# Kernel tuning notes

Hardware: AMD Instinct MI355X
Metric: run time of the kernel (lower is better)

Reference implementation:

```python
import jax, jax.numpy as jnp
import numpy as np

VOCABS = (30000, 20000, 10000, 8000, 5000, 30000, 20000, 10000)
OUT_LEN = 30000
D = 512
H = 4
DK = D // H
N_LAYERS = 4
DFF = 4 * D
BAT = 2048
S = 8


def _layernorm(x, a, b, eps=1e-6):
    # Annotated-transformer LayerNorm: a*(x-mean)/(std+eps)+b, unbiased std (torch default)
    mu = jnp.mean(x, axis=-1, keepdims=True)
    sd = jnp.std(x, axis=-1, ddof=1, keepdims=True)
    return a * (x - mu) / (sd + eps) + b


def setup_inputs() -> dict:
    key = jax.random.key(0)
    ks = jax.random.split(key, 32)
    sc = 0.02
    inp = {
        'sentence': jax.random.randint(ks[0], (BAT, S), 0, min(VOCABS)),
        'mask': jnp.ones((BAT, S), jnp.float32),
        'maskedIndex': jax.random.randint(ks[1], (BAT,), 0, S),
        # padded embedding tables (tied with decoder weights): [n_cols, OUT_LEN, D]
        'emb': jax.random.normal(ks[2], (S, OUT_LEN, D), jnp.float32) * sc,
        'dec_bias': jnp.zeros((S, OUT_LEN), jnp.float32),
        'Wq': jax.random.normal(ks[3], (N_LAYERS, D, D), jnp.float32) * sc,
        'bq': jnp.zeros((N_LAYERS, D), jnp.float32),
        'Wk': jax.random.normal(ks[4], (N_LAYERS, D, D), jnp.float32) * sc,
        'bk': jnp.zeros((N_LAYERS, D), jnp.float32),
        'Wv': jax.random.normal(ks[5], (N_LAYERS, D, D), jnp.float32) * sc,
        'bv': jnp.zeros((N_LAYERS, D), jnp.float32),
        'Wo': jax.random.normal(ks[6], (N_LAYERS, D, D), jnp.float32) * sc,
        'bo': jnp.zeros((N_LAYERS, D), jnp.float32),
        'W1': jax.random.normal(ks[7], (N_LAYERS, D, DFF), jnp.float32) * sc,
        'b1': jnp.zeros((N_LAYERS, DFF), jnp.float32),
        'W2': jax.random.normal(ks[8], (N_LAYERS, DFF, D), jnp.float32) * sc,
        'b2': jnp.zeros((N_LAYERS, D), jnp.float32),
        'ln1_a': jnp.ones((N_LAYERS, D), jnp.float32),
        'ln1_b': jnp.zeros((N_LAYERS, D), jnp.float32),
        'ln2_a': jnp.ones((N_LAYERS, D), jnp.float32),
        'ln2_b': jnp.zeros((N_LAYERS, D), jnp.float32),
        'fn_a': jnp.ones((D,), jnp.float32),
        'fn_b': jnp.zeros((D,), jnp.float32),
    }
    return inp


def reference(sentence, mask, maskedIndex, emb, dec_bias, Wq, bq, Wk, bk, Wv, bv,
              Wo, bo, W1, b1, W2, b2, ln1_a, ln1_b, ln2_a, ln2_b, fn_a, fn_b):
    B = sentence.shape[0]
    # per-column embedding lookup then concat along seq dim -> [B, S, D]
    x = jnp.stack([emb[k][sentence[:, k]] for k in range(S)], axis=1)
    # sinusoidal positional encoding (dropout p=0)
    pos = jnp.arange(S, dtype=jnp.float32)[:, None]
    div = jnp.exp(jnp.arange(0, D, 2, dtype=jnp.float32) * (-np.log(10000.0) / D))
    pe = jnp.zeros((S, D), jnp.float32)
    pe = pe.at[:, 0::2].set(jnp.sin(pos * div)).at[:, 1::2].set(jnp.cos(pos * div))
    x = x + pe[None]
    # mask: [B,S] -> unsqueeze(-1) -> unsqueeze(1) => [B,1,S,1], broadcast vs [B,h,S,S]
    mask_b = (mask[:, None, :, None] == 0)
    scale = 1.0 / np.sqrt(DK)
    for i in range(N_LAYERS):  # pre-LN encoder layers
        h = _layernorm(x, ln1_a[i], ln1_b[i])
        q = (h @ Wq[i] + bq[i]).reshape(B, S, H, DK)
        k = (h @ Wk[i] + bk[i]).reshape(B, S, H, DK)
        v = (h @ Wv[i] + bv[i]).reshape(B, S, H, DK)
        scores = jnp.einsum('bqhd,bkhd->bhqk', q, k) * scale
        scores = jnp.where(mask_b, -1e9, scores)
        p = jax.nn.softmax(scores, axis=-1)
        att = jnp.einsum('bhqk,bkhd->bqhd', p, v).reshape(B, S, D)
        x = x + att @ Wo[i] + bo[i]
        h2 = _layernorm(x, ln2_a[i], ln2_b[i])
        x = x + jax.nn.relu(h2 @ W1[i] + b1[i]) @ W2[i] + b2[i]
    out = _layernorm(x, fn_a, fn_b)
    # per-sample masked-token decode with tied embedding weights, -inf pad to OUT_LEN
    hsel = out[jnp.arange(B), maskedIndex]  # [B, D]
    neg = jnp.float32(-jnp.inf)
    preds = jnp.full((B, OUT_LEN), neg, dtype=out.dtype)
    for kc in range(S):
        vk = VOCABS[kc]
        logits = hsel @ emb[kc, :vk].T + dec_bias[kc, :vk]  # [B, vk]
        if vk < OUT_LEN:
            logits = jnp.concatenate(
                [logits, jnp.full((B, OUT_LEN - vk), neg, out.dtype)], axis=1)
        preds = jnp.where((maskedIndex == kc)[:, None], logits, preds)
    return preds
```

## Files before the change

### kernel.cpp

```cpp
#include <hip/hip_runtime.h>
#include <cstdint>

#define B_   2048
#define S_   8
#define D_   512
#define H_   4
#define DK_  128
#define NL_  4
#define DFF_ 2048
#define OUT_ 30000
#define SENTINEL_ (-1.0e30f)

typedef unsigned short ushort_t;
typedef __attribute__((ext_vector_type(8))) short bf16x8;
typedef __attribute__((ext_vector_type(4))) float f32x4;

__constant__ int VOC_[8] = {30000, 20000, 10000, 8000, 5000, 30000, 20000, 10000};

__device__ __forceinline__ ushort_t f2bf(float f) {
    union { float f; unsigned u; } x; x.f = f;
    unsigned r = x.u + 0x7fffu + ((x.u >> 16) & 1u);
    return (ushort_t)(r >> 16);
}
__device__ __forceinline__ float bf2f(ushort_t h) {
    union { unsigned u; float f; } x; x.u = (unsigned)h << 16;
    return x.f;
}

__global__ __launch_bounds__(256) void convw_k(const float* __restrict__ W,
                                               ushort_t* __restrict__ Wt,
                                               int K, int N) {
    const size_t mat = (size_t)K * N;
    const float* Wz = W + (size_t)blockIdx.z * mat;
    ushort_t* Wtz = Wt + (size_t)blockIdx.z * mat;
    __shared__ __align__(16) ushort_t t[32][40];
    int tid = threadIdx.x;
    int k0 = blockIdx.y * 32, n0 = blockIdx.x * 32;
    int r = tid >> 3, c4 = (tid & 7) * 4;
    float4 v = *(const float4*)(Wz + (size_t)(k0 + r) * N + n0 + c4);
    t[c4 + 0][r] = f2bf(v.x);
    t[c4 + 1][r] = f2bf(v.y);
    t[c4 + 2][r] = f2bf(v.z);
    t[c4 + 3][r] = f2bf(v.w);
    __syncthreads();
    int n = tid >> 3, q = tid & 7;
    uint2 d = *(uint2*)&t[n][q * 4];
    *(uint2*)(Wtz + (size_t)(n0 + n) * K + k0 + q * 4) = d;
}

__global__ __launch_bounds__(128) void embed_pe(const int* __restrict__ sent,
                                                const float* __restrict__ emb,
                                                float* __restrict__ x) {
    int row = blockIdx.x;
    int s = row & 7;
    int tok = sent[row];
    const float* e = emb + ((size_t)s * OUT_ + tok) * D_;
    int d0 = threadIdx.x * 4;
    float4 v = *(const float4*)(e + d0);
    float r[4] = {v.x, v.y, v.z, v.w};
#pragma unroll
    for (int i = 0; i < 4; ++i) {
        int d = d0 + i;
        int i2 = d & ~1;
        float dv = expf((float)i2 * (-9.210340371976184f / 512.f));
        float ang = (float)s * dv;
        r[i] += (d & 1) ? cosf(ang) : sinf(ang);
    }
    *(float4*)(x + (size_t)row * D_ + d0) = make_float4(r[0], r[1], r[2], r[3]);
}

__global__ __launch_bounds__(256) void layernorm_k(const float* __restrict__ x,
                                                   const float* __restrict__ ga,
                                                   const float* __restrict__ gb,
                                                   ushort_t* __restrict__ out) {
    int row  = blockIdx.x * 4 + (threadIdx.x >> 6);
    int lane = threadIdx.x & 63;
    const float* xr = x + (size_t)row * D_;
    float4 v0 = *(const float4*)(xr + lane * 8);
    float4 v1 = *(const float4*)(xr + lane * 8 + 4);
    float s = v0.x + v0.y + v0.z + v0.w + v1.x + v1.y + v1.z + v1.w;
#pragma unroll
    for (int m = 1; m < 64; m <<= 1) s += __shfl_xor(s, m);
    float mu = s * (1.f / 512.f);
    float d0 = v0.x - mu, d1 = v0.y - mu, d2 = v0.z - mu, d3 = v0.w - mu;
    float d4 = v1.x - mu, d5 = v1.y - mu, d6 = v1.z - mu, d7 = v1.w - mu;
    float sq = d0*d0 + d1*d1 + d2*d2 + d3*d3 + d4*d4 + d5*d5 + d6*d6 + d7*d7;
#pragma unroll
    for (int m = 1; m < 64; m <<= 1) sq += __shfl_xor(sq, m);
    float sd  = sqrtf(sq * (1.f / 511.f));
    float inv = 1.f / (sd + 1e-6f);
    float4 a0 = *(const float4*)(ga + lane * 8);
    float4 a1 = *(const float4*)(ga + lane * 8 + 4);
    float4 b0 = *(const float4*)(gb + lane * 8);
    float4 b1 = *(const float4*)(gb + lane * 8 + 4);
    ushort_t u[8];
    u[0] = f2bf(a0.x * d0 * inv + b0.x);  u[1] = f2bf(a0.y * d1 * inv + b0.y);
    u[2] = f2bf(a0.z * d2 * inv + b0.z);  u[3] = f2bf(a0.w * d3 * inv + b0.w);
    u[4] = f2bf(a1.x * d4 * inv + b1.x);  u[5] = f2bf(a1.y * d5 * inv + b1.y);
    u[6] = f2bf(a1.z * d6 * inv + b1.z);  u[7] = f2bf(a1.w * d7 * inv + b1.w);
    *(uint4*)(out + (size_t)row * D_ + lane * 8) = *(uint4*)u;
}

__global__ __launch_bounds__(256) void hsel_ln_k(const float* __restrict__ x,
                                                 const int* __restrict__ mi,
                                                 const float* __restrict__ ga,
                                                 const float* __restrict__ gb,
                                                 ushort_t* __restrict__ hsel) {
    int b    = blockIdx.x * 4 + (threadIdx.x >> 6);
    int lane = threadIdx.x & 63;
    const float* xr = x + ((size_t)b * S_ + mi[b]) * D_;
    float4 v0 = *(const float4*)(xr + lane * 8);
    float4 v1 = *(const float4*)(xr + lane * 8 + 4);
    float s = v0.x + v0.y + v0.z + v0.w + v1.x + v1.y + v1.z + v1.w;
#pragma unroll
    for (int m = 1; m < 64; m <<= 1) s += __shfl_xor(s, m);
    float mu = s * (1.f / 512.f);
    float d0 = v0.x - mu, d1 = v0.y - mu, d2 = v0.z - mu, d3 = v0.w - mu;
    float d4 = v1.x - mu, d5 = v1.y - mu, d6 = v1.z - mu, d7 = v1.w - mu;
    float sq = d0*d0 + d1*d1 + d2*d2 + d3*d3 + d4*d4 + d5*d5 + d6*d6 + d7*d7;
#pragma unroll
    for (int m = 1; m < 64; m <<= 1) sq += __shfl_xor(sq, m);
    float sd  = sqrtf(sq * (1.f / 511.f));
    float inv = 1.f / (sd + 1e-6f);
    float4 a0 = *(const float4*)(ga + lane * 8);
    float4 a1 = *(const float4*)(ga + lane * 8 + 4);
    float4 b0 = *(const float4*)(gb + lane * 8);
    float4 b1 = *(const float4*)(gb + lane * 8 + 4);
    ushort_t u[8];
    u[0] = f2bf(a0.x * d0 * inv + b0.x);  u[1] = f2bf(a0.y * d1 * inv + b0.y);
    u[2] = f2bf(a0.z * d2 * inv + b0.z);  u[3] = f2bf(a0.w * d3 * inv + b0.w);
    u[4] = f2bf(a1.x * d4 * inv + b1.x);  u[5] = f2bf(a1.y * d5 * inv + b1.y);
    u[6] = f2bf(a1.z * d6 * inv + b1.z);  u[7] = f2bf(a1.w * d7 * inv + b1.w);
    *(uint4*)(hsel + (size_t)b * D_ + lane * 8) = *(uint4*)u;
}

template<int RELU, int ACCF32>
__global__ __launch_bounds__(256) void gemm_bt(const ushort_t* __restrict__ A,
                                               const ushort_t* __restrict__ Bt,
                                               const float* __restrict__ bias,
                                               float* __restrict__ Cf,
                                               ushort_t* __restrict__ Cb,
                                               int M, int N, int K) {
    __shared__ __align__(16) ushort_t As[128][40];
    __shared__ __align__(16) ushort_t Bs[128][40];
    const int tid = threadIdx.x;
    const int m0 = blockIdx.y * 128, n0 = blockIdx.x * 128;
    const int lane = tid & 63, w = tid >> 6;
    const int wm = (w >> 1) * 64, wn = (w & 1) * 64;
    const int l15 = lane & 15, kg = lane >> 4;
    f32x4 acc[4][4] = {};
    for (int k0 = 0; k0 < K; k0 += 32) {
        __syncthreads();
#pragma unroll
        for (int it = 0; it < 2; ++it) {
            int lin = tid + it * 256;
            int r = lin >> 2, q = lin & 3;
            *(uint4*)&As[r][q * 8] =
                *(const uint4*)(A + (size_t)(m0 + r) * K + k0 + q * 8);
            *(uint4*)&Bs[r][q * 8] =
                *(const uint4*)(Bt + (size_t)(n0 + r) * K + k0 + q * 8);
        }
        __syncthreads();
        bf16x8 af[4], bfr[4];
#pragma unroll
        for (int m = 0; m < 4; ++m)
            af[m] = *(const bf16x8*)&As[wm + m * 16 + l15][kg * 8];
#pragma unroll
        for (int n = 0; n < 4; ++n)
            bfr[n] = *(const bf16x8*)&Bs[wn + n * 16 + l15][kg * 8];
#pragma unroll
        for (int m = 0; m < 4; ++m)
#pragma unroll
            for (int n = 0; n < 4; ++n)
                acc[m][n] = __builtin_amdgcn_mfma_f32_16x16x32_bf16(
                    af[m], bfr[n], acc[m][n], 0, 0, 0);
    }
#pragma unroll
    for (int n = 0; n < 4; ++n) {
        int col = n0 + wn + n * 16 + l15;
        float bv = bias[col];
#pragma unroll
        for (int m = 0; m < 4; ++m) {
            int rbase = m0 + wm + m * 16 + kg * 4;
#pragma unroll
            for (int r = 0; r < 4; ++r) {
                float v = acc[m][n][r] + bv;
                if (RELU) v = fmaxf(v, 0.f);
                size_t idx = (size_t)(rbase + r) * N + col;
                if (ACCF32) Cf[idx] += v;
                else        Cb[idx] = f2bf(v);
            }
        }
    }
}

__global__ __launch_bounds__(256) void attn_k(const ushort_t* __restrict__ q,
                                              const ushort_t* __restrict__ k,
                                              const ushort_t* __restrict__ v,
                                              const float* __restrict__ mask,
                                              ushort_t* __restrict__ att) {
    int b = blockIdx.x;
    __shared__ float qs[S_][D_], ks[S_][D_], vs[S_][D_];
    __shared__ float ps[H_][S_][S_];
    const int tid = threadIdx.x;
#pragma unroll
    for (int it = 0; it < 2; ++it) {
        int lin = tid + it * 256;
        int s = lin >> 6, d8 = (lin & 63) * 8;
        size_t g = ((size_t)b * S_ + s) * D_ + d8;
        union { uint4 u4; ushort_t u[8]; } uq, uk, uv;
        uq.u4 = *(const uint4*)(q + g);
        uk.u4 = *(const uint4*)(k + g);
        uv.u4 = *(const uint4*)(v + g);
#pragma unroll
        for (int i = 0; i < 8; ++i) {
            qs[s][d8 + i] = bf2f(uq.u[i]);
            ks[s][d8 + i] = bf2f(uk.u[i]);
            vs[s][d8 + i] = bf2f(uv.u[i]);
        }
    }
    __syncthreads();
    const int hh = tid >> 6, lane = tid & 63;
    const int qq = lane >> 3, kk = lane & 7;
    const int off = hh * DK_;
    float s = 0.f;
#pragma unroll
    for (int d = 0; d < DK_; ++d) s = fmaf(qs[qq][off + d], ks[kk][off + d], s);
    s *= 0.08838834764831845f;
    if (mask[b * S_ + qq] == 0.f) s = -1e9f;
    float mx = s;
#pragma unroll
    for (int m = 1; m < 8; m <<= 1) mx = fmaxf(mx, __shfl_xor(mx, m, 8));
    float e = expf(s - mx);
    float sum = e;
#pragma unroll
    for (int m = 1; m < 8; m <<= 1) sum += __shfl_xor(sum, m, 8);
    ps[hh][qq][kk] = e / sum;
    __syncthreads();
#pragma unroll
    for (int q2 = 0; q2 < 8; ++q2) {
        float a0 = 0.f, a1 = 0.f;
#pragma unroll
        for (int k2 = 0; k2 < 8; ++k2) {
            float p = ps[hh][q2][k2];
            a0 = fmaf(p, vs[k2][off + lane], a0);
            a1 = fmaf(p, vs[k2][off + 64 + lane], a1);
        }
        size_t g = ((size_t)b * S_ + q2) * D_ + off;
        att[g + lane]      = f2bf(a0);
        att[g + 64 + lane] = f2bf(a1);
    }
}

__global__ __launch_bounds__(256) void compact_k(const int* __restrict__ mi,
                                                 int* __restrict__ idxg,
                                                 int* __restrict__ off) {
    __shared__ int cnt[8], pos[9];
    int tid = threadIdx.x;
    if (tid < 8) cnt[tid] = 0;
    __syncthreads();
    for (int i = tid; i < B_; i += 256) atomicAdd(&cnt[mi[i]], 1);
    __syncthreads();
    if (tid == 0) {
        pos[0] = 0;
        for (int kc = 0; kc < 8; ++kc) pos[kc + 1] = pos[kc] + cnt[kc];
        for (int kc = 0; kc < 9; ++kc) off[kc] = pos[kc];
    }
    __syncthreads();
    if (tid < 8) cnt[tid] = pos[tid];
    __syncthreads();
    for (int i = tid; i < B_; i += 256) {
        int p = atomicAdd(&cnt[mi[i]], 1);
        idxg[p] = i;
    }
}

__global__ __launch_bounds__(256) void decode_mfma(const ushort_t* __restrict__ hselb,
                                                   const float* __restrict__ emb,
                                                   const float* __restrict__ dbias,
                                                   const int* __restrict__ idxg,
                                                   const int* __restrict__ offg,
                                                   float* __restrict__ out) {
    const int kc = blockIdx.y;
    const int base = offg[kc];
    const int Mg = offg[kc + 1] - base;
    const int m0 = blockIdx.z * 256;
    if (m0 >= Mg) return;
    const int j0 = blockIdx.x * 64;
    const int vk = VOC_[kc];
    const int tid = threadIdx.x;
    const int lane = tid & 63, w = tid >> 6;
    const int l15 = lane & 15, kg = lane >> 4;
    const int wm = w * 64;
    const float* et = emb + (size_t)kc * OUT_ * D_;
    __shared__ __align__(16) ushort_t As[256][40];
    __shared__ __align__(16) ushort_t Bs[64][40];
    f32x4 acc[4][4] = {};
    const bool act = (j0 < vk);
    if (act) {
        for (int k0 = 0; k0 < 512; k0 += 32) {
            __syncthreads();
#pragma unroll
            for (int it = 0; it < 4; ++it) {
                int lin = tid + it * 256;
                int r = lin >> 2, qq = lin & 3;
                uint4 va = make_uint4(0u, 0u, 0u, 0u);
                int m = m0 + r;
                if (m < Mg) {
                    int gb = idxg[base + m];
                    va = *(const uint4*)(hselb + (size_t)gb * D_ + k0 + qq * 8);
                }
                *(uint4*)&As[r][qq * 8] = va;
            }
            {
                int j = tid >> 2, qq = tid & 3;
                int jj = j0 + j; if (jj >= vk) jj = vk - 1;
                const float* src = et + (size_t)jj * D_ + k0 + qq * 8;
                float4 f0 = *(const float4*)src;
                float4 f1 = *(const float4*)(src + 4);
                ushort_t u[8] = {f2bf(f0.x), f2bf(f0.y), f2bf(f0.z), f2bf(f0.w),
                                 f2bf(f1.x), f2bf(f1.y), f2bf(f1.z), f2bf(f1.w)};
                *(uint4*)&Bs[j][qq * 8] = *(uint4*)u;
            }
            __syncthreads();
            bf16x8 af[4], bfr[4];
#pragma unroll
            for (int m = 0; m < 4; ++m)
                af[m] = *(const bf16x8*)&As[wm + m * 16 + l15][kg * 8];
#pragma unroll
            for (int n = 0; n < 4; ++n)
                bfr[n] = *(const bf16x8*)&Bs[n * 16 + l15][kg * 8];
#pragma unroll
            for (int m = 0; m < 4; ++m)
#pragma unroll
                for (int n = 0; n < 4; ++n)
                    acc[m][n] = __builtin_amdgcn_mfma_f32_16x16x32_bf16(
                        af[m], bfr[n], acc[m][n], 0, 0, 0);
        }
    }
#pragma unroll
    for (int m = 0; m < 4; ++m) {
        int rbase = m0 + wm + m * 16 + kg * 4;
#pragma unroll
        for (int r = 0; r < 4; ++r) {
            int mm = rbase + r;
            if (mm >= Mg) continue;
            int b = idxg[base + mm];
            float* orow = out + (size_t)b * OUT_;
#pragma unroll
            for (int n = 0; n < 4; ++n) {
                int col = j0 + n * 16 + l15;
                if (col >= OUT_) continue;
                float v = SENTINEL_;
                if (act && col < vk)
                    v = acc[m][n][r] + dbias[kc * OUT_ + col];
                orow[col] = v;
            }
        }
    }
}

extern "C" void kernel_launch(void* const* d_in, const int* in_sizes, int n_in,
                              void* d_out, int out_size, void* d_ws, size_t ws_size,
                              hipStream_t stream) {
    const int*   sent  = (const int*)d_in[0];
    const float* mask  = (const float*)d_in[1];
    const int*   mi    = (const int*)d_in[2];
    const float* emb   = (const float*)d_in[3];
    const float* dbias = (const float*)d_in[4];
    const float* Wq = (const float*)d_in[5],  *bq = (const float*)d_in[6];
    const float* Wk = (const float*)d_in[7],  *bk = (const float*)d_in[8];
    const float* Wv = (const float*)d_in[9],  *bv = (const float*)d_in[10];
    const float* Wo = (const float*)d_in[11], *bo = (const float*)d_in[12];
    const float* W1 = (const float*)d_in[13], *b1 = (const float*)d_in[14];
    const float* W2 = (const float*)d_in[15], *b2 = (const float*)d_in[16];
    const float* ln1_a = (const float*)d_in[17], *ln1_b = (const float*)d_in[18];
    const float* ln2_a = (const float*)d_in[19], *ln2_b = (const float*)d_in[20];
    const float* fn_a  = (const float*)d_in[21], *fn_b  = (const float*)d_in[22];
    float* out = (float*)d_out;

    const size_t NX = (size_t)B_ * S_ * D_;
    char* p = (char*)d_ws;
    float*    x     = (float*)p;      p += NX * 4;
    ushort_t* h     = (ushort_t*)p;   p += NX * 2;
    ushort_t* reg   = (ushort_t*)p;   p += 4 * NX * 2;
    ushort_t* qb2   = reg;
    ushort_t* kb2   = reg + NX;
    ushort_t* vb2   = reg + 2 * NX;
    ushort_t* ffn1  = reg;
    const size_t WSQ = (size_t)NL_ * D_ * D_;
    const size_t WFF = (size_t)NL_ * D_ * DFF_;
    ushort_t* WqT = (ushort_t*)p;  p += WSQ * 2;
    ushort_t* WkT = (ushort_t*)p;  p += WSQ * 2;
    ushort_t* WvT = (ushort_t*)p;  p += WSQ * 2;
    ushort_t* WoT = (ushort_t*)p;  p += WSQ * 2;
    ushort_t* W1T = (ushort_t*)p;  p += WFF * 2;
    ushort_t* W2T = (ushort_t*)p;  p += WFF * 2;
    ushort_t* hselb = (ushort_t*)p; p += (size_t)B_ * D_ * 2;
    int* idxg = (int*)p;  p += B_ * 4;
    int* offg = (int*)p;

    const int ROWS = B_ * S_;

    convw_k<<<dim3(16, 16, NL_), 256, 0, stream>>>(Wq, WqT, D_, D_);
    convw_k<<<dim3(16, 16, NL_), 256, 0, stream>>>(Wk, WkT, D_, D_);
    convw_k<<<dim3(16, 16, NL_), 256, 0, stream>>>(Wv, WvT, D_, D_);
    convw_k<<<dim3(16, 16, NL_), 256, 0, stream>>>(Wo, WoT, D_, D_);
    convw_k<<<dim3(64, 16, NL_), 256, 0, stream>>>(W1, W1T, D_, DFF_);
    convw_k<<<dim3(16, 64, NL_), 256, 0, stream>>>(W2, W2T, DFF_, D_);

    embed_pe<<<ROWS, 128, 0, stream>>>(sent, emb, x);

    for (int L = 0; L < NL_; ++L) {
        layernorm_k<<<ROWS / 4, 256, 0, stream>>>(x, ln1_a + L * D_, ln1_b + L * D_, h);
        gemm_bt<0, 0><<<dim3(D_ / 128, ROWS / 128), 256, 0, stream>>>(
            h, WqT + (size_t)L * D_ * D_, bq + L * D_, nullptr, qb2, ROWS, D_, D_);
        gemm_bt<0, 0><<<dim3(D_ / 128, ROWS / 128), 256, 0, stream>>>(
            h, WkT + (size_t)L * D_ * D_, bk + L * D_, nullptr, kb2, ROWS, D_, D_);
        gemm_bt<0, 0><<<dim3(D_ / 128, ROWS / 128), 256, 0, stream>>>(
            h, WvT + (size_t)L * D_ * D_, bv + L * D_, nullptr, vb2, ROWS, D_, D_);
        attn_k<<<B_, 256, 0, stream>>>(qb2, kb2, vb2, mask, h);
        gemm_bt<0, 1><<<dim3(D_ / 128, ROWS / 128), 256, 0, stream>>>(
            h, WoT + (size_t)L * D_ * D_, bo + L * D_, x, nullptr, ROWS, D_, D_);
        layernorm_k<<<ROWS / 4, 256, 0, stream>>>(x, ln2_a + L * D_, ln2_b + L * D_, h);
        gemm_bt<1, 0><<<dim3(DFF_ / 128, ROWS / 128), 256, 0, stream>>>(
            h, W1T + (size_t)L * D_ * DFF_, b1 + L * DFF_, nullptr, ffn1, ROWS, DFF_, D_);
        gemm_bt<0, 1><<<dim3(D_ / 128, ROWS / 128), 256, 0, stream>>>(
            ffn1, W2T + (size_t)L * DFF_ * D_, b2 + L * D_, x, nullptr, ROWS, D_, DFF_);
    }

    hsel_ln_k<<<B_ / 4, 256, 0, stream>>>(x, mi, fn_a, fn_b, hselb);
    compact_k<<<1, 256, 0, stream>>>(mi, idxg, offg);
    decode_mfma<<<dim3((OUT_ + 63) / 64, 8, 2), 256, 0, stream>>>(
        hselb, emb, dbias, idxg, offg, out);
}
```

Before: 2.036 ms.

## Fuse QKV GEMMs, use direct global-to-LDS loads, pre-gather decode rows

Concatenates the Q, K and V weights and biases so one GEMM with N=1536 writes an interleaved qkv buffer that attention reads directly. It replaces register-staged tile loads in the GEMM and decode kernels with global_load_lds into unpadded LDS tiles. The final layernorm now writes hidden rows already grouped by column through a rank array, so decode can load A tiles directly. Decode also prefetches the next embedding chunk into registers. Dropping the LDS padding may add bank conflicts on the fragment reads, and it adds a small bias-fusion kernel.

```diff
diff --git a/kernel.cpp b/kernel.cpp
--- a/kernel.cpp
+++ b/kernel.cpp
@@ -27,12 +27,15 @@
     return x.f;
 }
 
+#define GLOAD_LDS16(g, l) __builtin_amdgcn_global_load_lds( \
+    (const __attribute__((address_space(1))) void*)(g),     \
+    (__attribute__((address_space(3))) void*)(l), 16, 0, 0)
+
 __global__ __launch_bounds__(256) void convw_k(const float* __restrict__ W,
                                                ushort_t* __restrict__ Wt,
-                                               int K, int N) {
-    const size_t mat = (size_t)K * N;
-    const float* Wz = W + (size_t)blockIdx.z * mat;
-    ushort_t* Wtz = Wt + (size_t)blockIdx.z * mat;
+                                               int K, int N, size_t ostride) {
+    const float* Wz = W + (size_t)blockIdx.z * K * N;
+    ushort_t* Wtz = Wt + (size_t)blockIdx.z * ostride;
     __shared__ __align__(16) ushort_t t[32][40];
     int tid = threadIdx.x;
     int k0 = blockIdx.y * 32, n0 = blockIdx.x * 32;
@@ -46,6 +49,18 @@
     int n = tid >> 3, q = tid & 7;
     uint2 d = *(uint2*)&t[n][q * 4];
     *(uint2*)(Wtz + (size_t)(n0 + n) * K + k0 + q * 4) = d;
+}
+
+__global__ __launch_bounds__(256) void biasfuse_k(const float* __restrict__ bq,
+                                                  const float* __restrict__ bk,
+                                                  const float* __restrict__ bv,
+                                                  float* __restrict__ o) {
+    int i = blockIdx.x * 256 + threadIdx.x;
+    int L = i / 1536, c = i % 1536;
+    float v = (c < 512) ? bq[L * 512 + c]
+            : (c < 1024) ? bk[L * 512 + c - 512]
+                         : bv[L * 512 + c - 1024];
+    o[i] = v;
 }
 
 __global__ __launch_bounds__(128) void embed_pe(const int* __restrict__ sent,
@@ -103,9 +118,10 @@
 
 __global__ __launch_bounds__(256) void hsel_ln_k(const float* __restrict__ x,
                                                  const int* __restrict__ mi,
+                                                 const int* __restrict__ rank,
                                                  const float* __restrict__ ga,
                                                  const float* __restrict__ gb,
-                                                 ushort_t* __restrict__ hsel) {
+                                                 ushort_t* __restrict__ hselg) {
     int b    = blockIdx.x * 4 + (threadIdx.x >> 6);
     int lane = threadIdx.x & 63;
     const float* xr = x + ((size_t)b * S_ + mi[b]) * D_;
@@ -131,7 +147,7 @@
     u[2] = f2bf(a0.z * d2 * inv + b0.z);  u[3] = f2bf(a0.w * d3 * inv + b0.w);
     u[4] = f2bf(a1.x * d4 * inv + b1.x);  u[5] = f2bf(a1.y * d5 * inv + b1.y);
     u[6] = f2bf(a1.z * d6 * inv + b1.z);  u[7] = f2bf(a1.w * d7 * inv + b1.w);
-    *(uint4*)(hsel + (size_t)b * D_ + lane * 8) = *(uint4*)u;
+    *(uint4*)(hselg + (size_t)rank[b] * D_ + lane * 8) = *(uint4*)u;
 }
 
 template<int RELU, int ACCF32>
@@ -141,33 +157,34 @@
                                                float* __restrict__ Cf,
                                                ushort_t* __restrict__ Cb,
                                                int M, int N, int K) {
-    __shared__ __align__(16) ushort_t As[128][40];
-    __shared__ __align__(16) ushort_t Bs[128][40];
+    __shared__ __align__(16) ushort_t As[128 * 32];
+    __shared__ __align__(16) ushort_t Bs[128 * 32];
     const int tid = threadIdx.x;
     const int m0 = blockIdx.y * 128, n0 = blockIdx.x * 128;
     const int lane = tid & 63, w = tid >> 6;
     const int wm = (w >> 1) * 64, wn = (w & 1) * 64;
     const int l15 = lane & 15, kg = lane >> 4;
+    const int srow = tid >> 2, scq8 = (tid & 3) * 8;
+    const ushort_t* ga0 = A  + (size_t)(m0 + srow) * K + scq8;
+    const ushort_t* gb0 = Bt + (size_t)(n0 + srow) * K + scq8;
+    ushort_t* lA0 = As + w * 64 * 8;
+    ushort_t* lB0 = Bs + w * 64 * 8;
     f32x4 acc[4][4] = {};
     for (int k0 = 0; k0 < K; k0 += 32) {
         __syncthreads();
 #pragma unroll
         for (int it = 0; it < 2; ++it) {
-            int lin = tid + it * 256;
-            int r = lin >> 2, q = lin & 3;
-            *(uint4*)&As[r][q * 8] =
-                *(const uint4*)(A + (size_t)(m0 + r) * K + k0 + q * 8);
-            *(uint4*)&Bs[r][q * 8] =
-                *(const uint4*)(Bt + (size_t)(n0 + r) * K + k0 + q * 8);
+            GLOAD_LDS16(ga0 + (size_t)it * 64 * K + k0, lA0 + it * 2048);
+            GLOAD_LDS16(gb0 + (size_t)it * 64 * K + k0, lB0 + it * 2048);
         }
         __syncthreads();
         bf16x8 af[4], bfr[4];
 #pragma unroll
         for (int m = 0; m < 4; ++m)
-            af[m] = *(const bf16x8*)&As[wm + m * 16 + l15][kg * 8];
+            af[m] = *(const bf16x8*)(As + (wm + m * 16 + l15) * 32 + kg * 8);
 #pragma unroll
         for (int n = 0; n < 4; ++n)
-            bfr[n] = *(const bf16x8*)&Bs[wn + n * 16 + l15][kg * 8];
+            bfr[n] = *(const bf16x8*)(Bs + (wn + n * 16 + l15) * 32 + kg * 8);
 #pragma unroll
         for (int m = 0; m < 4; ++m)
 #pragma unroll
@@ -194,9 +211,7 @@
     }
 }
 
-__global__ __launch_bounds__(256) void attn_k(const ushort_t* __restrict__ q,
-                                              const ushort_t* __restrict__ k,
-                                              const ushort_t* __restrict__ v,
+__global__ __launch_bounds__(256) void attn_k(const ushort_t* __restrict__ qkv,
                                               const float* __restrict__ mask,
                                               ushort_t* __restrict__ att) {
     int b = blockIdx.x;
@@ -207,11 +222,11 @@
     for (int it = 0; it < 2; ++it) {
         int lin = tid + it * 256;
         int s = lin >> 6, d8 = (lin & 63) * 8;
-        size_t g = ((size_t)b * S_ + s) * D_ + d8;
+        size_t rb = ((size_t)b * S_ + s) * 1536 + d8;
         union { uint4 u4; ushort_t u[8]; } uq, uk, uv;
-        uq.u4 = *(const uint4*)(q + g);
-        uk.u4 = *(const uint4*)(k + g);
-        uv.u4 = *(const uint4*)(v + g);
+        uq.u4 = *(const uint4*)(qkv + rb);
+        uk.u4 = *(const uint4*)(qkv + rb + 512);
+        uv.u4 = *(const uint4*)(qkv + rb + 1024);
 #pragma unroll
         for (int i = 0; i < 8; ++i) {
             qs[s][d8 + i] = bf2f(uq.u[i]);
@@ -254,6 +269,7 @@
 
 __global__ __launch_bounds__(256) void compact_k(const int* __restrict__ mi,
                                                  int* __restrict__ idxg,
+                                                 int* __restrict__ rank,
                                                  int* __restrict__ off) {
     __shared__ int cnt[8], pos[9];
     int tid = threadIdx.x;
@@ -272,10 +288,11 @@
     for (int i = tid; i < B_; i += 256) {
         int p = atomicAdd(&cnt[mi[i]], 1);
         idxg[p] = i;
-    }
-}
-
-__global__ __launch_bounds__(256) void decode_mfma(const ushort_t* __restrict__ hselb,
+        rank[i] = p;
+    }
+}
+
+__global__ __launch_bounds__(256) void decode_mfma(const ushort_t* __restrict__ hselg,
                                                    const float* __restrict__ emb,
                                                    const float* __restrict__ dbias,
                                                    const int* __restrict__ idxg,
@@ -292,44 +309,40 @@
     const int lane = tid & 63, w = tid >> 6;
     const int l15 = lane & 15, kg = lane >> 4;
     const int wm = w * 64;
-    const float* et = emb + (size_t)kc * OUT_ * D_;
-    __shared__ __align__(16) ushort_t As[256][40];
-    __shared__ __align__(16) ushort_t Bs[64][40];
+    __shared__ __align__(16) ushort_t As[256 * 32];
+    __shared__ __align__(16) ushort_t Bs[64 * 32];
     f32x4 acc[4][4] = {};
     const bool act = (j0 < vk);
     if (act) {
+        const int srow = tid >> 2, scq8 = (tid & 3) * 8;
+        const ushort_t* gA0 = hselg + (size_t)(base + m0 + srow) * D_ + scq8;
+        ushort_t* lA0 = As + w * 64 * 8;
+        int jj = j0 + srow; if (jj >= vk) jj = vk - 1;
+        const float* gB = emb + ((size_t)kc * OUT_ + jj) * D_ + scq8;
+        float4 e0 = *(const float4*)(gB);
+        float4 e1 = *(const float4*)(gB + 4);
         for (int k0 = 0; k0 < 512; k0 += 32) {
             __syncthreads();
 #pragma unroll
-            for (int it = 0; it < 4; ++it) {
-                int lin = tid + it * 256;
-                int r = lin >> 2, qq = lin & 3;
-                uint4 va = make_uint4(0u, 0u, 0u, 0u);
-                int m = m0 + r;
-                if (m < Mg) {
-                    int gb = idxg[base + m];
-                    va = *(const uint4*)(hselb + (size_t)gb * D_ + k0 + qq * 8);
-                }
-                *(uint4*)&As[r][qq * 8] = va;
+            for (int it = 0; it < 4; ++it)
+                GLOAD_LDS16(gA0 + (size_t)it * 64 * D_ + k0, lA0 + it * 2048);
+            {
+                ushort_t u[8] = {f2bf(e0.x), f2bf(e0.y), f2bf(e0.z), f2bf(e0.w),
+                                 f2bf(e1.x), f2bf(e1.y), f2bf(e1.z), f2bf(e1.w)};
+                *(uint4*)(Bs + srow * 32 + scq8) = *(uint4*)u;
             }
-            {
-                int j = tid >> 2, qq = tid & 3;
-                int jj = j0 + j; if (jj >= vk) jj = vk - 1;
-                const float* src = et + (size_t)jj * D_ + k0 + qq * 8;
-                float4 f0 = *(const float4*)src;
-                float4 f1 = *(const float4*)(src + 4);
-                ushort_t u[8] = {f2bf(f0.x), f2bf(f0.y), f2bf(f0.z), f2bf(f0.w),
-                                 f2bf(f1.x), f2bf(f1.y), f2bf(f1.z), f2bf(f1.w)};
-                *(uint4*)&Bs[j][qq * 8] = *(uint4*)u;
+            if (k0 + 32 < 512) {
+                e0 = *(const float4*)(gB + k0 + 32);
+                e1 = *(const float4*)(gB + k0 + 36);
             }
             __syncthreads();
             bf16x8 af[4], bfr[4];
 #pragma unroll
             for (int m = 0; m < 4; ++m)
-                af[m] = *(const bf16x8*)&As[wm + m * 16 + l15][kg * 8];
+                af[m] = *(const bf16x8*)(As + (wm + m * 16 + l15) * 32 + kg * 8);
 #pragma unroll
             for (int n = 0; n < 4; ++n)
-                bfr[n] = *(const bf16x8*)&Bs[n * 16 + l15][kg * 8];
+                bfr[n] = *(const bf16x8*)(Bs + (n * 16 + l15) * 32 + kg * 8);
 #pragma unroll
             for (int m = 0; m < 4; ++m)
 #pragma unroll
@@ -380,57 +393,55 @@
     float* out = (float*)d_out;
 
     const size_t NX = (size_t)B_ * S_ * D_;
+    const size_t DD = (size_t)D_ * D_;
     char* p = (char*)d_ws;
     float*    x     = (float*)p;      p += NX * 4;
     ushort_t* h     = (ushort_t*)p;   p += NX * 2;
-    ushort_t* reg   = (ushort_t*)p;   p += 4 * NX * 2;
-    ushort_t* qb2   = reg;
-    ushort_t* kb2   = reg + NX;
-    ushort_t* vb2   = reg + 2 * NX;
-    ushort_t* ffn1  = reg;
-    const size_t WSQ = (size_t)NL_ * D_ * D_;
-    const size_t WFF = (size_t)NL_ * D_ * DFF_;
-    ushort_t* WqT = (ushort_t*)p;  p += WSQ * 2;
-    ushort_t* WkT = (ushort_t*)p;  p += WSQ * 2;
-    ushort_t* WvT = (ushort_t*)p;  p += WSQ * 2;
-    ushort_t* WoT = (ushort_t*)p;  p += WSQ * 2;
-    ushort_t* W1T = (ushort_t*)p;  p += WFF * 2;
-    ushort_t* W2T = (ushort_t*)p;  p += WFF * 2;
-    ushort_t* hselb = (ushort_t*)p; p += (size_t)B_ * D_ * 2;
+    ushort_t* big   = (ushort_t*)p;   p += (size_t)B_ * S_ * DFF_ * 2;
+    ushort_t* qkvb  = big;
+    ushort_t* ffn1  = big;
+    ushort_t* WqkvT = (ushort_t*)p;  p += (size_t)NL_ * 3 * DD * 2;
+    ushort_t* WoT   = (ushort_t*)p;  p += (size_t)NL_ * DD * 2;
+    ushort_t* W1T   = (ushort_t*)p;  p += (size_t)NL_ * D_ * DFF_ * 2;
+    ushort_t* W2T   = (ushort_t*)p;  p += (size_t)NL_ * DFF_ * D_ * 2;
+    float*    bqkv  = (float*)p;     p += (size_t)NL_ * 1536 * 4;
+    ushort_t* hselg = (ushort_t*)p;  p += (size_t)(B_ + 256) * D_ * 2;
     int* idxg = (int*)p;  p += B_ * 4;
+    int* rank = (int*)p;  p += B_ * 4;
     int* offg = (int*)p;
 
     const int ROWS = B_ * S_;
 
-    convw_k<<<dim3(16, 16, NL_), 256, 0, stream>>>(Wq, WqT, D_, D_);
-    convw_k<<<dim3(16, 16, NL_), 256, 0, stream>>>(Wk, WkT, D_, D_);
-    convw_k<<<dim3(16, 16, NL_), 256, 0, stream>>>(Wv, WvT, D_, D_);
-    convw_k<<<dim3(16, 16, NL_), 256, 0, stream>>>(Wo, WoT, D_, D_);
-    convw_k<<<dim3(64, 16, NL_), 256, 0, stream>>>(W1, W1T, D_, DFF_);
-    convw_k<<<dim3(16, 64, NL_), 256, 0, stream>>>(W2, W2T, DFF_, D_);
+    compact_k<<<1, 256, 0, stream>>>(mi, idxg, rank, offg);
+
+    convw_k<<<dim3(16, 16, NL_), 256, 0, stream>>>(Wq, WqkvT,          D_, D_, 3 * DD);
+    convw_k<<<dim3(16, 16, NL_), 256, 0, stream>>>(Wk, WqkvT + DD,     D_, D_, 3 * DD);
+    convw_k<<<dim3(16, 16, NL_), 256, 0, stream>>>(Wv, WqkvT + 2 * DD, D_, D_, 3 * DD);
+    convw_k<<<dim3(16, 16, NL_), 256, 0, stream>>>(Wo, WoT, D_, D_, DD);
+    convw_k<<<dim3(64, 16, NL_), 256, 0, stream>>>(W1, W1T, D_, DFF_, (size_t)D_ * DFF_);
+    convw_k<<<dim3(16, 64, NL_), 256, 0, stream>>>(W2, W2T, DFF_, D_, (size_t)DFF_ * D_);
+    biasfuse_k<<<24, 256, 0, stream>>>(bq, bk, bv, bqkv);
 
     embed_pe<<<ROWS, 128, 0, stream>>>(sent, emb, x);
 
     for (int L = 0; L < NL_; ++L) {
         layernorm_k<<<ROWS / 4, 256, 0, stream>>>(x, ln1_a + L * D_, ln1_b + L * D_, h);
-        gemm_bt<0, 0><<<dim3(D_ / 128, ROWS / 128), 256, 0, stream>>>(
-            h, WqT + (size_t)L * D_ * D_, bq + L * D_, nullptr, qb2, ROWS, D_, D_);
-        gemm_bt<0, 0><<<dim3(D_ / 128, ROWS / 128), 256, 0, stream>>>(
-            h, WkT + (size_t)L * D_ * D_, bk + L * D_, nullptr, kb2, ROWS, D_, D_);
-        gemm_bt<0, 0><<<dim3(D_ / 128, ROWS / 128), 256, 0, stream>>>(
-            h, WvT + (size_t)L * D_ * D_, bv + L * D_, nullptr, vb2, ROWS, D_, D_);
-        attn_k<<<B_, 256, 0, stream>>>(qb2, kb2, vb2, mask, h);
-        gemm_bt<0, 1><<<dim3(D_ / 128, ROWS / 128), 256, 0, stream>>>(
-            h, WoT + (size_t)L * D_ * D_, bo + L * D_, x, nullptr, ROWS, D_, D_);
+        gemm_bt<0, 0><<<dim3(12, ROWS / 128), 256, 0, stream>>>(
+            h, WqkvT + (size_t)L * 3 * DD, bqkv + L * 1536, nullptr, qkvb,
+            ROWS, 1536, D_);
+        attn_k<<<B_, 256, 0, stream>>>(qkvb, mask, h);
+        gemm_bt<0, 1><<<dim3(4, ROWS / 128), 256, 0, stream>>>(
+            h, WoT + (size_t)L * DD, bo + L * D_, x, nullptr, ROWS, D_, D_);
         layernorm_k<<<ROWS / 4, 256, 0, stream>>>(x, ln2_a + L * D_, ln2_b + L * D_, h);
-        gemm_bt<1, 0><<<dim3(DFF_ / 128, ROWS / 128), 256, 0, stream>>>(
-            h, W1T + (size_t)L * D_ * DFF_, b1 + L * DFF_, nullptr, ffn1, ROWS, DFF_, D_);
-        gemm_bt<0, 1><<<dim3(D_ / 128, ROWS / 128), 256, 0, stream>>>(
-            ffn1, W2T + (size_t)L * DFF_ * D_, b2 + L * D_, x, nullptr, ROWS, D_, DFF_);
-    }
-
-    hsel_ln_k<<<B_ / 4, 256, 0, stream>>>(x, mi, fn_a, fn_b, hselb);
-    compact_k<<<1, 256, 0, stream>>>(mi, idxg, offg);
+        gemm_bt<1, 0><<<dim3(16, ROWS / 128), 256, 0, stream>>>(
+            h, W1T + (size_t)L * D_ * DFF_, b1 + L * DFF_, nullptr, ffn1,
+            ROWS, DFF_, D_);
+        gemm_bt<0, 1><<<dim3(4, ROWS / 128), 256, 0, stream>>>(
+            ffn1, W2T + (size_t)L * DFF_ * D_, b2 + L * D_, x, nullptr,
+            ROWS, D_, DFF_);
+    }
+
+    hsel_ln_k<<<B_ / 4, 256, 0, stream>>>(x, mi, rank, fn_a, fn_b, hselg);
     decode_mfma<<<dim3((OUT_ + 63) / 64, 8, 2), 256, 0, stream>>>(
-        hselb, emb, dbias, idxg, offg, out);
-}
+        hselg, emb, dbias, idxg, offg, out);
+}
```

Measured after the change: 1.908 ms. -6.3%, faster.
